# Kernel optimization log

Hardware: AMD Instinct MI355X
Metric: run time of the kernel (lower is better)

Reference implementation:

```python
import jax, jax.numpy as jnp
import numpy as np
import math

NB_STEPS = 50

def compute_cc_weights(nb_steps):
    # Faithful port of the torch/numpy Clenshaw-Curtis weight construction.
    lam = np.arange(0, nb_steps + 1, 1).reshape(-1, 1)
    lam = np.cos(lam @ lam.T * math.pi / nb_steps)
    lam[:, 0] = 0.5
    lam[:, -1] = 0.5 * lam[:, -1]
    lam = lam * 2 / nb_steps
    W = np.arange(0, nb_steps + 1, 1).reshape(-1, 1)
    W[np.arange(1, nb_steps + 1, 2)] = 0
    W = 2 / (1 - W ** 2)
    W[0] = 1
    W[np.arange(1, nb_steps + 1, 2)] = 0
    cc_weights = (lam.T @ W).astype(np.float32)  # [S+1, 1]
    steps = np.cos(np.arange(0, nb_steps + 1, 1).reshape(-1, 1) * math.pi / nb_steps).astype(np.float32)  # [S+1, 1]
    return jnp.asarray(cc_weights)[:, 0], jnp.asarray(steps)[:, 0]

CC_W, CC_S = compute_cc_weights(NB_STEPS)

def setup_inputs() -> dict:
    key = jax.random.key(0)
    k1, k2, k3, k4, k5 = jax.random.split(key, 5)
    H = 128
    bound1 = 1.0  # Linear(1,H): fan_in=1 -> kaiming-uniform-ish bound
    bound2 = 1.0 / math.sqrt(H)
    return {
        "x": jax.random.normal(k1, (256, 128), dtype=jnp.float32),
        "W1": jax.random.uniform(k2, (H, 1), jnp.float32, -bound1, bound1),
        "b1": jax.random.uniform(k3, (H,), jnp.float32, -bound1, bound1),
        "W2": jax.random.uniform(k4, (1, H), jnp.float32, -bound2, bound2),
        "b2": jax.random.uniform(k5, (1,), jnp.float32, -bound2, bound2),
    }

def _integrand(X, W1, b1, W2, b2):
    # X: [..., 1] -> scalar output per point; Linear(1,H)+ReLU+Linear(H,1)+ELU+1
    h = jax.nn.relu(X * W1[:, 0] + b1)          # [..., H]
    f = jnp.einsum('...h,h->...', h, W2[0]) + b2[0]
    return jax.nn.elu(f) + 1.0                   # positive transform

def reference(x, W1, b1, W2, b2):
    shape = x.shape
    xf = x.reshape(-1, 1)                        # [N, 1], x0 = 0
    # Quadrature nodes: x0 + (xT - x0) * (s + 1)/2 with x0 = 0, xT = x
    X_steps = xf * ((CC_S + 1.0) * 0.5)          # [N, S+1]
    dzs = _integrand(X_steps[..., None], W1, b1, W2, b2)  # [N, S+1]
    z = jnp.einsum('ns,s->n', dzs, CC_W)         # weighted sum over nodes
    z = z * (xf[:, 0] * 0.5)                     # * (xT - x0) / 2
    return z.reshape(shape)
```

## Files before the change

### kernel.cpp

```cpp
#include <hip/hip_runtime.h>
#include <math.h>

#define NB 50
#define NS 52
#define H  128
#define SPT 13

__global__ __launch_bounds__(256) void umnn_kernel(
    const float* __restrict__ x,
    const float* __restrict__ W1,
    const float* __restrict__ b1,
    const float* __restrict__ W2,
    const float* __restrict__ b2,
    float* __restrict__ out,
    int N)
{
    __shared__ float s_w1[H], s_b1[H], s_w2[H];
    __shared__ float s_ccw[NS], s_ccs[NS];

    const int tid = threadIdx.x;

    if (tid < H) {
        s_w1[tid] = W1[tid];
        s_b1[tid] = b1[tid];
        s_w2[tid] = W2[tid];
    }

    if (tid < NS) {
        const int s = tid;
        if (s <= NB) {
            s_ccs[s] = cosf((float)s * ((float)M_PI / (float)NB));
            float sum = 0.0f;
            for (int k = 0; k <= NB; k += 2) {
                float L;
                if (s == 0)       L = 0.5f;
                else if (s == NB) L = 0.5f;
                else              L = cosf((float)(k * s) * ((float)M_PI / (float)NB));
                const float Wk = (k == 0) ? 1.0f : 2.0f / (1.0f - (float)(k * k));
                sum += L * Wk;
            }
            s_ccw[s] = sum * (2.0f / (float)NB);
        } else {
            s_ccs[s] = 0.0f;
            s_ccw[s] = 0.0f;
        }
    }
    __syncthreads();

    const int g     = blockIdx.x * blockDim.x + tid;
    const int n     = g >> 2;
    const int chunk = g & 3;
    if (n >= N) return;

    const float xf  = x[n];
    const float b2v = b2[0];
    const int   s0  = chunk * SPT;

    float Xs[SPT], acc[SPT];
#pragma unroll
    for (int i = 0; i < SPT; ++i) {
        Xs[i]  = xf * (s_ccs[s0 + i] + 1.0f) * 0.5f;
        acc[i] = 0.0f;
    }

#pragma unroll 2
    for (int j = 0; j < H; ++j) {
        const float w1 = s_w1[j];
        const float bb = s_b1[j];
        const float w2 = s_w2[j];
#pragma unroll
        for (int i = 0; i < SPT; ++i) {
            float h = fmaf(Xs[i], w1, bb);
            h = fmaxf(h, 0.0f);
            acc[i] = fmaf(h, w2, acc[i]);
        }
    }

    float z = 0.0f;
#pragma unroll
    for (int i = 0; i < SPT; ++i) {
        const float f = acc[i] + b2v;
        const float e = (f > 0.0f) ? f : (__expf(f) - 1.0f);
        z = fmaf(e + 1.0f, s_ccw[s0 + i], z);
    }

    z += __shfl_xor(z, 1);
    z += __shfl_xor(z, 2);
    if (chunk == 0) out[n] = z * xf * 0.5f;
}

extern "C" void kernel_launch(void* const* d_in, const int* in_sizes, int n_in,
                              void* d_out, int out_size, void* d_ws, size_t ws_size,
                              hipStream_t stream) {
    const float* x  = (const float*)d_in[0];
    const float* W1 = (const float*)d_in[1];
    const float* b1 = (const float*)d_in[2];
    const float* W2 = (const float*)d_in[3];
    const float* b2 = (const float*)d_in[4];
    float* out = (float*)d_out;

    const int N = in_sizes[0];
    const int threads = 256;
    const int total   = N * 4;
    const int blocks  = (total + threads - 1) / threads;

    umnn_kernel<<<blocks, threads, 0, stream>>>(x, W1, b1, W2, b2, out, N);
}
```

Measured before the change: 83.62 us.

## Replace hidden-layer loop with piecewise-linear breakpoint search and prefix sums

Treats the ReLU MLP as a piecewise-linear function of the scalar input. Each block sorts the 128 breakpoints by rank counting, builds prefix sums of slope and intercept, and each quadrature node then does a binary search plus one FMA instead of a 128-step loop. This removes the O(H) per-node arithmetic but adds per-block sort/scan setup, several extra barriers and data-dependent shared-memory gathers. Fast __cosf is also used for the weight setup, which may slightly change precision.

```diff
diff --git a/kernel.cpp b/kernel.cpp
--- a/kernel.cpp
+++ b/kernel.cpp
@@ -1,12 +1,13 @@
 #include <hip/hip_runtime.h>
 #include <math.h>
+#include <float.h>
 
 #define NB 50
 #define NS 52
 #define H  128
 #define SPT 13
 
-__global__ __launch_bounds__(256) void umnn_kernel(
+__global__ __launch_bounds__(256) void umnn_pw(
     const float* __restrict__ x,
     const float* __restrict__ W1,
     const float* __restrict__ b1,
@@ -15,28 +16,49 @@
     float* __restrict__ out,
     int N)
 {
-    __shared__ float s_w1[H], s_b1[H], s_w2[H];
+    __shared__ __align__(16) float s_tmp[H];
+    __shared__ float s_t[2 * H];
+    __shared__ float s_dA[H], s_dB[H];
+    __shared__ float s_pA[H + 1], s_pB[H + 1];
     __shared__ float s_ccw[NS], s_ccs[NS];
+    __shared__ float s_red[8];
 
     const int tid = threadIdx.x;
 
+    float t = 0.0f, dA = 0.0f, dB = 0.0f;
     if (tid < H) {
-        s_w1[tid] = W1[tid];
-        s_b1[tid] = b1[tid];
-        s_w2[tid] = W2[tid];
-    }
-
-    if (tid < NS) {
-        const int s = tid;
+        const float w1 = W1[tid];
+        const float bb = b1[tid];
+        const float w2 = W2[tid];
+        const bool zero = (w1 == 0.0f);
+        t = zero ? FLT_MAX : (-bb / w1);
+        const float sgn = (w1 > 0.0f) ? 1.0f : -1.0f;
+        dA = zero ? 0.0f : sgn * w2 * w1;
+        dB = zero ? 0.0f : sgn * w2 * bb;
+        float baseA = (w1 < 0.0f) ? w2 * w1 : 0.0f;
+        float baseB = (w1 < 0.0f) ? w2 * bb : (zero ? w2 * fmaxf(bb, 0.0f) : 0.0f);
+        s_tmp[tid] = t;
+        s_t[H + tid] = FLT_MAX;
+#pragma unroll
+        for (int off = 1; off < 64; off <<= 1) {
+            baseA += __shfl_xor(baseA, off);
+            baseB += __shfl_xor(baseB, off);
+        }
+        if ((tid & 63) == 0) {
+            s_red[(tid >> 6) * 2 + 0] = baseA;
+            s_red[(tid >> 6) * 2 + 1] = baseB;
+        }
+    } else if (tid < H + NS) {
+        const int s = tid - H;
         if (s <= NB) {
-            s_ccs[s] = cosf((float)s * ((float)M_PI / (float)NB));
+            s_ccs[s] = __cosf((float)s * ((float)M_PI / (float)NB));
             float sum = 0.0f;
-            for (int k = 0; k <= NB; k += 2) {
+            for (int kk = 0; kk <= NB; kk += 2) {
                 float L;
                 if (s == 0)       L = 0.5f;
                 else if (s == NB) L = 0.5f;
-                else              L = cosf((float)(k * s) * ((float)M_PI / (float)NB));
-                const float Wk = (k == 0) ? 1.0f : 2.0f / (1.0f - (float)(k * k));
+                else              L = __cosf((float)(kk * s) * ((float)M_PI / (float)NB));
+                const float Wk = (kk == 0) ? 1.0f : 2.0f / (1.0f - (float)(kk * kk));
                 sum += L * Wk;
             }
             s_ccw[s] = sum * (2.0f / (float)NB);
@@ -47,8 +69,54 @@
     }
     __syncthreads();
 
-    const int g     = blockIdx.x * blockDim.x + tid;
-    const int n     = g >> 2;
+    if (tid < H) {
+        const float4* t4 = (const float4*)s_tmp;
+        int rank = 0;
+#pragma unroll 8
+        for (int j4 = 0; j4 < H / 4; ++j4) {
+            const float4 v = t4[j4];
+            const int jb = 4 * j4;
+            rank += (v.x < t) || (v.x == t && (jb + 0) < tid);
+            rank += (v.y < t) || (v.y == t && (jb + 1) < tid);
+            rank += (v.z < t) || (v.z == t && (jb + 2) < tid);
+            rank += (v.w < t) || (v.w == t && (jb + 3) < tid);
+        }
+        s_t[rank]  = t;
+        s_dA[rank] = dA;
+        s_dB[rank] = dB;
+    }
+    __syncthreads();
+
+    float sa = 0.0f, sb = 0.0f;
+    if (tid < H) {
+        sa = s_dA[tid];
+        sb = s_dB[tid];
+        const int lane = tid & 63;
+#pragma unroll
+        for (int off = 1; off < 64; off <<= 1) {
+            const float ta = __shfl_up(sa, off);
+            const float tb = __shfl_up(sb, off);
+            if (lane >= off) { sa += ta; sb += tb; }
+        }
+        if (lane == 63) {
+            s_red[4 + (tid >> 6) * 2] = sa;
+            s_red[5 + (tid >> 6) * 2] = sb;
+        }
+    }
+    __syncthreads();
+    if (tid < H) {
+        const float A0 = s_red[0] + s_red[2];
+        const float B0 = s_red[1] + s_red[3];
+        const float addA = A0 + ((tid >= 64) ? s_red[4] : 0.0f);
+        const float addB = B0 + ((tid >= 64) ? s_red[5] : 0.0f);
+        s_pA[tid + 1] = sa + addA;
+        s_pB[tid + 1] = sb + addB;
+        if (tid == 0) { s_pA[0] = A0; s_pB[0] = B0; }
+    }
+    __syncthreads();
+
+    const int g = blockIdx.x * blockDim.x + tid;
+    const int n = g >> 2;
     const int chunk = g & 3;
     if (n >= N) return;
 
@@ -56,30 +124,26 @@
     const float b2v = b2[0];
     const int   s0  = chunk * SPT;
 
-    float Xs[SPT], acc[SPT];
+    float Xi[SPT];
+    int   k[SPT];
 #pragma unroll
     for (int i = 0; i < SPT; ++i) {
-        Xs[i]  = xf * (s_ccs[s0 + i] + 1.0f) * 0.5f;
-        acc[i] = 0.0f;
+        Xi[i] = xf * (s_ccs[s0 + i] + 1.0f) * 0.5f;
+        k[i]  = 0;
     }
-
-#pragma unroll 2
-    for (int j = 0; j < H; ++j) {
-        const float w1 = s_w1[j];
-        const float bb = s_b1[j];
-        const float w2 = s_w2[j];
+#pragma unroll
+    for (int st = 128; st >= 1; st >>= 1) {
 #pragma unroll
         for (int i = 0; i < SPT; ++i) {
-            float h = fmaf(Xs[i], w1, bb);
-            h = fmaxf(h, 0.0f);
-            acc[i] = fmaf(h, w2, acc[i]);
+            k[i] += (s_t[k[i] + st - 1] < Xi[i]) ? st : 0;
         }
     }
-
     float z = 0.0f;
 #pragma unroll
     for (int i = 0; i < SPT; ++i) {
-        const float f = acc[i] + b2v;
+        const float A = s_pA[k[i]];
+        const float B = s_pB[k[i]];
+        const float f = fmaf(A, Xi[i], B) + b2v;
         const float e = (f > 0.0f) ? f : (__expf(f) - 1.0f);
         z = fmaf(e + 1.0f, s_ccw[s0 + i], z);
     }
@@ -101,8 +165,8 @@
 
     const int N = in_sizes[0];
     const int threads = 256;
-    const int total   = N * 4;
-    const int blocks  = (total + threads - 1) / threads;
+    const int total = N * 4;
+    const int blocks = (total + threads - 1) / threads;
 
-    umnn_kernel<<<blocks, threads, 0, stream>>>(x, W1, b1, W2, b2, out, N);
+    umnn_pw<<<blocks, threads, 0, stream>>>(x, W1, b1, W2, b2, out, N);
 }
```

Measured after the change: 69.38 us. 17.0% less time.
